# Performance work log

Measured on AMD Instinct MI355X. Metric: run time of the kernel, lower is better.

## Reference

```python
import jax, jax.numpy as jnp
import numpy as np

DIM = 1024
H = 16
DH = 64
INTER = H * DH

def setup_inputs() -> dict:
    key = jax.random.key(0)
    k1, k2, k3, k4 = jax.random.split(key, 4)
    input = jax.random.normal(k1, (4, 2048, DIM), dtype=jnp.float32)
    # nn.Linear weights stored as [out, in]; we keep [in, out] for x @ W
    W_qkv = jax.random.normal(k2, (DIM, INTER * 3), dtype=jnp.float32) * 0.02
    W_mlp = jax.random.normal(k3, (INTER, DIM), dtype=jnp.float32) * 0.02
    b_mlp = jax.random.normal(k4, (DIM,), dtype=jnp.float32) * 0.02
    return {"input": input, "W_qkv": W_qkv, "W_mlp": W_mlp, "b_mlp": b_mlp}

def reference(input, W_qkv, W_mlp, b_mlp):
    b, n, _ = input.shape
    qkv = input @ W_qkv                      # [b, n, 3*h*d]
    qkv = qkv.reshape(b, n, 3, H, DH)        # matches '(qkv h d)' split order
    qkv = jnp.transpose(qkv, (2, 0, 3, 1, 4))  # [3, b, h, n, d]
    q, k, v = qkv[0], qkv[1], qkv[2]
    scale = DH ** -0.5
    attn = jnp.einsum('bhnd,bhmd->bhnm', q, k) * scale
    attn = jax.nn.softmax(attn, axis=-1)
    out = jnp.einsum('bhnm,bhmd->bhnd', attn, v)
    out = jnp.transpose(out, (0, 2, 1, 3)).reshape(b, n, INTER)  # 'b h n d -> b n (h d)'
    return out @ W_mlp + b_mlp
```

## Files before the change

### kernel.cpp

```cpp
#include <hip/hip_runtime.h>
#include <stdint.h>

typedef __attribute__((ext_vector_type(8))) short bf16x8;
typedef __attribute__((ext_vector_type(4))) float f32x4;
typedef __attribute__((ext_vector_type(16))) float f32x16;

#define MFMA16(a, b, c) __builtin_amdgcn_mfma_f32_16x16x32_bf16((a), (b), (c), 0, 0, 0)
#define MFMA32(a, b, c) __builtin_amdgcn_mfma_f32_32x32x16_bf16((a), (b), (c), 0, 0, 0)

__device__ __forceinline__ unsigned short f2bf(float x) {
  uint32_t u = __float_as_uint(x);
  u += 0x7fffu + ((u >> 16) & 1u);
  return (unsigned short)(u >> 16);
}

__device__ __forceinline__ uint32_t cvt_pk_bf16(float a, float b) {
  uint32_t r;
  asm("v_cvt_pk_bf16_f32 %0, %1, %2" : "=v"(r) : "v"(a), "v"(b));
  return r;
}

__device__ __forceinline__ float exp2_hw(float x) {
  float r;
  asm("v_exp_f32 %0, %1" : "=v"(r) : "v"(x));
  return r;
}

__device__ __forceinline__ void gload_lds16(const void* g, void* l) {
  __builtin_amdgcn_global_load_lds(
      (const __attribute__((address_space(1))) uint32_t*)g,
      (__attribute__((address_space(3))) uint32_t*)l, 16, 0, 0);
}

__global__ __launch_bounds__(256) void prep_kernel(
    const float* __restrict__ X, unsigned short* __restrict__ Xb,
    const float* __restrict__ Wq, unsigned short* __restrict__ Wqt,
    const float* __restrict__ Wm, unsigned short* __restrict__ Wmt) {
  __shared__ float tile[64][65];
  const int bid = blockIdx.x;
  const int t = threadIdx.x;
  if (bid < 4096) {
    const int i = bid * 256 + t;
    const float4 a = *(const float4*)(X + (size_t)i * 8);
    const float4 b = *(const float4*)(X + (size_t)i * 8 + 4);
    uint4 o;
    o.x = (uint32_t)f2bf(a.x) | ((uint32_t)f2bf(a.y) << 16);
    o.y = (uint32_t)f2bf(a.z) | ((uint32_t)f2bf(a.w) << 16);
    o.z = (uint32_t)f2bf(b.x) | ((uint32_t)f2bf(b.y) << 16);
    o.w = (uint32_t)f2bf(b.z) | ((uint32_t)f2bf(b.w) << 16);
    *(uint4*)(Xb + (size_t)i * 8) = o;
    return;
  }
  const float* src;
  unsigned short* dst;
  int Nd, lb;
  if (bid < 4864) { src = Wq; dst = Wqt; Nd = 3072; lb = bid - 4096; }
  else            { src = Wm; dst = Wmt; Nd = 1024; lb = bid - 4864; }
  const int Kd = 1024;
  const int ntc = Nd >> 6;
  const int r0 = (lb / ntc) << 6;
  const int c0 = (lb % ntc) << 6;
  const int tr = t >> 4;
  const int tc4 = (t & 15) << 2;
#pragma unroll
  for (int p = 0; p < 4; ++p) {
    int row = p * 16 + tr;
    float4 v = *(const float4*)(src + (size_t)(r0 + row) * Nd + c0 + tc4);
    tile[row][tc4 + 0] = v.x;
    tile[row][tc4 + 1] = v.y;
    tile[row][tc4 + 2] = v.z;
    tile[row][tc4 + 3] = v.w;
  }
  __syncthreads();
#pragma unroll
  for (int p = 0; p < 4; ++p) {
    int c = p * 16 + tr;
    int r4 = (t & 15) << 2;
    uint2 pv;
    pv.x = (uint32_t)f2bf(tile[r4 + 0][c]) | ((uint32_t)f2bf(tile[r4 + 1][c]) << 16);
    pv.y = (uint32_t)f2bf(tile[r4 + 2][c]) | ((uint32_t)f2bf(tile[r4 + 3][c]) << 16);
    *(uint2*)(dst + (size_t)(c0 + c) * Kd + r0 + r4) = pv;
  }
}

__global__ __launch_bounds__(256) void gemm_qkv_kernel(
    const unsigned short* __restrict__ A,
    const unsigned short* __restrict__ Bt,
    unsigned short* __restrict__ Qo,
    unsigned short* __restrict__ Ko,
    unsigned short* __restrict__ Vo) {
  constexpr int Kdim = 1024, BK = 64;
  __shared__ unsigned short lA[128 * BK];
  __shared__ unsigned short lB[128 * BK];
  const int nbn = 24;
  const int wg = (blockIdx.x & 7) * 192 + (blockIdx.x >> 3);
  const int bi = wg / nbn, bj = wg % nbn;
  const int tid = threadIdx.x;
  const int l = tid & 63, w = tid >> 6;
  const int wr = w >> 1, wc = w & 1;
  const int lr = l & 15, lg = l >> 4;

  const f32x4 vzero = {0.f, 0.f, 0.f, 0.f};
  f32x4 acc[4][4];
#pragma unroll
  for (int i = 0; i < 4; ++i)
#pragma unroll
    for (int j = 0; j < 4; ++j) acc[i][j] = vzero;

  const int srow = tid >> 3;
  const int sc = tid & 7;
  const int sg = sc ^ (srow & 7);
  const unsigned short* As = A + (size_t)(bi * 128 + srow) * Kdim + sg * 8;
  const unsigned short* Bs = Bt + (size_t)(bj * 128 + srow) * Kdim + sg * 8;
  unsigned short* dA = &lA[(srow * 8 + sc) * 8];
  unsigned short* dB = &lB[(srow * 8 + sc) * 8];

  for (int kt = 0; kt < Kdim / BK; ++kt) {
    const int k0 = kt * BK;
#pragma unroll
    for (int rr = 0; rr < 4; ++rr) {
      gload_lds16(As + (size_t)rr * 32 * Kdim + k0, dA + rr * 32 * BK);
      gload_lds16(Bs + (size_t)rr * 32 * Kdim + k0, dB + rr * 32 * BK);
    }
    __syncthreads();
#pragma unroll
    for (int kk = 0; kk < 2; ++kk) {
      bf16x8 af[4], bfr[4];
#pragma unroll
      for (int it = 0; it < 4; ++it) {
        int r = wr * 64 + it * 16 + lr;
        af[it] = *(const bf16x8*)&lA[r * BK + (((kk * 4 + lg) ^ (lr & 7)) * 8)];
      }
#pragma unroll
      for (int jt = 0; jt < 4; ++jt) {
        int r = wc * 64 + jt * 16 + lr;
        bfr[jt] = *(const bf16x8*)&lB[r * BK + (((kk * 4 + lg) ^ (lr & 7)) * 8)];
      }
#pragma unroll
      for (int it = 0; it < 4; ++it)
#pragma unroll
        for (int jt = 0; jt < 4; ++jt)
          acc[it][jt] = MFMA16(af[it], bfr[jt], acc[it][jt]);
    }
    __syncthreads();
  }

#pragma unroll
  for (int jt = 0; jt < 4; ++jt) {
    const int col = bj * 128 + wc * 64 + jt * 16 + lr;
    const int s = col >> 10;
    const int rem = col & 1023;
    const int h = rem >> 6, d = rem & 63;
#pragma unroll
    for (int it = 0; it < 4; ++it) {
      const int m0 = bi * 128 + wr * 64 + it * 16 + lg * 4;
      const int b = m0 >> 11, n = m0 & 2047;
      const size_t bh = (size_t)b * 16 + h;
      if (s == 2) {
        uint2 pv;
        pv.x = (uint32_t)f2bf(acc[it][jt][0]) | ((uint32_t)f2bf(acc[it][jt][1]) << 16);
        pv.y = (uint32_t)f2bf(acc[it][jt][2]) | ((uint32_t)f2bf(acc[it][jt][3]) << 16);
        *(uint2*)(Vo + ((bh * 256 + (n >> 3)) * 64 + d) * 8 + (n & 7)) = pv;
      } else if (s == 1) {
        const size_t base = ((bh * 8 + (d >> 3)) * 2048) * 8 + (d & 7);
#pragma unroll
        for (int rg = 0; rg < 4; ++rg)
          Ko[base + (size_t)(n + rg) * 8] = f2bf(acc[it][jt][rg]);
      } else {
#pragma unroll
        for (int rg = 0; rg < 4; ++rg)
          Qo[(bh * 2048 + (size_t)(n + rg)) * 64 + d] = f2bf(acc[it][jt][rg] * 0.18033688011112042f);
      }
    }
  }
}

template <int T>
__device__ __forceinline__ bf16x8 build_pa(const f32x16& s, int hi) {
  uint32_t A1 = cvt_pk_bf16(s[T * 8 + 0], s[T * 8 + 1]);
  uint32_t A2 = cvt_pk_bf16(s[T * 8 + 2], s[T * 8 + 3]);
  uint32_t B1 = cvt_pk_bf16(s[T * 8 + 4], s[T * 8 + 5]);
  uint32_t B2 = cvt_pk_bf16(s[T * 8 + 6], s[T * 8 + 7]);
  uint32_t send1 = hi ? A1 : B1;
  uint32_t send2 = hi ? A2 : B2;
  uint32_t recv1 = (uint32_t)__shfl_xor((int)send1, 32);
  uint32_t recv2 = (uint32_t)__shfl_xor((int)send2, 32);
  union { uint32_t u[4]; bf16x8 v; } r;
  r.u[0] = hi ? recv1 : A1;
  r.u[1] = hi ? recv2 : A2;
  r.u[2] = hi ? B1 : recv1;
  r.u[3] = hi ? B2 : recv2;
  return r.v;
}

__device__ __forceinline__ float tile_sum(const f32x16& a, const f32x16& b) {
  float st[8];
#pragma unroll
  for (int i = 0; i < 8; ++i) st[i] = (a[i] + a[i + 8]) + (b[i] + b[i + 8]);
  float sm = ((st[0] + st[1]) + (st[2] + st[3])) + ((st[4] + st[5]) + (st[6] + st[7]));
  sm += __shfl_xor(sm, 32);
  return sm;
}

__global__ __launch_bounds__(256, 2) void attn_kernel(
    const unsigned short* __restrict__ Qg,
    const unsigned short* __restrict__ Kg,
    const unsigned short* __restrict__ Vg,
    unsigned short* __restrict__ AO) {
  const int bid = blockIdx.x;
  const int bh = (bid & 7) * 8 + (bid >> 6);
  const int qt = (bid >> 3) & 7;
  const int tid = threadIdx.x;
  const int l = tid & 63, w = tid >> 6;
  const int lo = l & 31, hi = l >> 5;
  const int qb = qt * 256 + w * 64;

  bf16x8 qfA[4], qfB[4];
  {
    const unsigned short* qrowA = Qg + ((size_t)bh * 2048 + qb + lo) * 64 + hi * 8;
    const unsigned short* qrowB = qrowA + 32 * 64;
#pragma unroll
    for (int ds = 0; ds < 4; ++ds) {
      qfA[ds] = *(const bf16x8*)(qrowA + ds * 16);
      qfB[ds] = *(const bf16x8*)(qrowB + ds * 16);
    }
  }

  f32x16 oA0, oA1, oB0, oB1;
#pragma unroll
  for (int i = 0; i < 16; ++i) { oA0[i] = 0.f; oA1[i] = 0.f; oB0[i] = 0.f; oB1[i] = 0.f; }
  float lA_ = 0.f, lB_ = 0.f;

  const unsigned short* Kp = Kg + ((size_t)(bh * 8 + hi) * 2048 + lo) * 8;
  const unsigned short* Vp = Vg + ((size_t)(bh * 256 + hi) * 64 + lo) * 8;

  bf16x8 kf0[4], kf1[4], vf0[4], vf1[4];
#pragma unroll
  for (int ds = 0; ds < 4; ++ds) {
    kf0[ds] = *(const bf16x8*)(Kp + ds * 32768);
    kf1[ds] = *(const bf16x8*)(Kp + ds * 32768 + 256);
  }

  for (int t = 0; t < 32; ++t) {
#pragma unroll
    for (int ks = 0; ks < 4; ++ks) {
      vf0[ks] = *(const bf16x8*)(Vp + (size_t)t * 4096 + ks * 1024);
      vf1[ks] = *(const bf16x8*)(Vp + (size_t)t * 4096 + ks * 1024 + 256);
    }

    f32x16 sA0, sA1, sB0, sB1;
#pragma unroll
    for (int i = 0; i < 16; ++i) { sA0[i] = 0.f; sA1[i] = 0.f; sB0[i] = 0.f; sB1[i] = 0.f; }
    __builtin_amdgcn_s_setprio(1);
#pragma unroll
    for (int ds = 0; ds < 4; ++ds) {
      sA0 = MFMA32(kf0[ds], qfA[ds], sA0);
      sA1 = MFMA32(kf1[ds], qfA[ds], sA1);
      sB0 = MFMA32(kf0[ds], qfB[ds], sB0);
      sB1 = MFMA32(kf1[ds], qfB[ds], sB1);
    }
    __builtin_amdgcn_s_setprio(0);

    if (t < 31) {
#pragma unroll
      for (int ds = 0; ds < 4; ++ds) {
        kf0[ds] = *(const bf16x8*)(Kp + (size_t)(t + 1) * 512 + ds * 32768);
        kf1[ds] = *(const bf16x8*)(Kp + (size_t)(t + 1) * 512 + ds * 32768 + 256);
      }
    }

#pragma unroll
    for (int i = 0; i < 16; ++i) { sA0[i] = exp2_hw(sA0[i]); sA1[i] = exp2_hw(sA1[i]); }
#pragma unroll
    for (int i = 0; i < 16; ++i) { sB0[i] = exp2_hw(sB0[i]); sB1[i] = exp2_hw(sB1[i]); }
    lA_ += tile_sum(sA0, sA1);
    lB_ += tile_sum(sB0, sB1);

    bf16x8 paA[4] = {build_pa<0>(sA0, hi), build_pa<1>(sA0, hi),
                     build_pa<0>(sA1, hi), build_pa<1>(sA1, hi)};
    bf16x8 paB[4] = {build_pa<0>(sB0, hi), build_pa<1>(sB0, hi),
                     build_pa<0>(sB1, hi), build_pa<1>(sB1, hi)};

    __builtin_amdgcn_s_setprio(1);
#pragma unroll
    for (int ks = 0; ks < 4; ++ks) {
      oA0 = MFMA32(vf0[ks], paA[ks], oA0);
      oA1 = MFMA32(vf1[ks], paA[ks], oA1);
      oB0 = MFMA32(vf0[ks], paB[ks], oB0);
      oB1 = MFMA32(vf1[ks], paB[ks], oB1);
    }
    __builtin_amdgcn_s_setprio(0);
  }

  const float linvA = 1.0f / lA_;
  const float linvB = 1.0f / lB_;
  const int b = bh >> 4, h = bh & 15;
  unsigned short* dstA = AO + ((size_t)(b * 2048 + qb + lo) * 1024 + h * 64 + 4 * hi);
  unsigned short* dstB = dstA + (size_t)32 * 1024;
#pragma unroll
  for (int q4 = 0; q4 < 4; ++q4) {
    uint2 p0;
    p0.x = cvt_pk_bf16(oA0[q4 * 4 + 0] * linvA, oA0[q4 * 4 + 1] * linvA);
    p0.y = cvt_pk_bf16(oA0[q4 * 4 + 2] * linvA, oA0[q4 * 4 + 3] * linvA);
    *(uint2*)(dstA + q4 * 8) = p0;
    uint2 p1;
    p1.x = cvt_pk_bf16(oA1[q4 * 4 + 0] * linvA, oA1[q4 * 4 + 1] * linvA);
    p1.y = cvt_pk_bf16(oA1[q4 * 4 + 2] * linvA, oA1[q4 * 4 + 3] * linvA);
    *(uint2*)(dstA + 32 + q4 * 8) = p1;
    uint2 p2;
    p2.x = cvt_pk_bf16(oB0[q4 * 4 + 0] * linvB, oB0[q4 * 4 + 1] * linvB);
    p2.y = cvt_pk_bf16(oB0[q4 * 4 + 2] * linvB, oB0[q4 * 4 + 3] * linvB);
    *(uint2*)(dstB + q4 * 8) = p2;
    uint2 p3;
    p3.x = cvt_pk_bf16(oB1[q4 * 4 + 0] * linvB, oB1[q4 * 4 + 1] * linvB);
    p3.y = cvt_pk_bf16(oB1[q4 * 4 + 2] * linvB, oB1[q4 * 4 + 3] * linvB);
    *(uint2*)(dstB + 32 + q4 * 8) = p3;
  }
}

__global__ __launch_bounds__(256) void gemm_mlp_kernel(
    const unsigned short* __restrict__ A,
    const unsigned short* __restrict__ Bt,
    const float* __restrict__ bias,
    float* __restrict__ out) {
  constexpr int Kdim = 1024, BK = 64;
  __shared__ unsigned short lA[128 * BK];
  __shared__ unsigned short lB[128 * BK];
  const int nbn = 8;
  const int wg = (blockIdx.x & 7) * 64 + (blockIdx.x >> 3);
  const int bi = wg / nbn, bj = wg % nbn;
  const int tid = threadIdx.x;
  const int l = tid & 63, w = tid >> 6;
  const int wr = w >> 1, wc = w & 1;
  const int lr = l & 15, lg = l >> 4;

  const f32x4 vzero = {0.f, 0.f, 0.f, 0.f};
  f32x4 acc[4][4];
#pragma unroll
  for (int i = 0; i < 4; ++i)
#pragma unroll
    for (int j = 0; j < 4; ++j) acc[i][j] = vzero;

  const int srow = tid >> 3;
  const int sc = tid & 7;
  const int sg = sc ^ (srow & 7);
  const unsigned short* As = A + (size_t)(bi * 128 + srow) * Kdim + sg * 8;
  const unsigned short* Bs = Bt + (size_t)(bj * 128 + srow) * Kdim + sg * 8;
  unsigned short* dA = &lA[(srow * 8 + sc) * 8];
  unsigned short* dB = &lB[(srow * 8 + sc) * 8];

  for (int kt = 0; kt < Kdim / BK; ++kt) {
    const int k0 = kt * BK;
#pragma unroll
    for (int rr = 0; rr < 4; ++rr) {
      gload_lds16(As + (size_t)rr * 32 * Kdim + k0, dA + rr * 32 * BK);
      gload_lds16(Bs + (size_t)rr * 32 * Kdim + k0, dB + rr * 32 * BK);
    }
    __syncthreads();
#pragma unroll
    for (int kk = 0; kk < 2; ++kk) {
      bf16x8 af[4], bfr[4];
#pragma unroll
      for (int it = 0; it < 4; ++it) {
        int r = wr * 64 + it * 16 + lr;
        af[it] = *(const bf16x8*)&lA[r * BK + (((kk * 4 + lg) ^ (lr & 7)) * 8)];
      }
#pragma unroll
      for (int jt = 0; jt < 4; ++jt) {
        int r = wc * 64 + jt * 16 + lr;
        bfr[jt] = *(const bf16x8*)&lB[r * BK + (((kk * 4 + lg) ^ (lr & 7)) * 8)];
      }
#pragma unroll
      for (int it = 0; it < 4; ++it)
#pragma unroll
        for (int jt = 0; jt < 4; ++jt)
          acc[it][jt] = MFMA16(af[it], bfr[jt], acc[it][jt]);
    }
    __syncthreads();
  }

#pragma unroll
  for (int jt = 0; jt < 4; ++jt) {
    const int col = bj * 128 + wc * 64 + jt * 16 + lr;
    const float bv = bias[col];
#pragma unroll
    for (int it = 0; it < 4; ++it) {
      const int m0 = bi * 128 + wr * 64 + it * 16 + lg * 4;
#pragma unroll
      for (int rg = 0; rg < 4; ++rg)
        out[(size_t)(m0 + rg) * 1024 + col] = acc[it][jt][rg] + bv;
    }
  }
}

extern "C" void kernel_launch(void* const* d_in, const int* in_sizes, int n_in,
                              void* d_out, int out_size, void* d_ws, size_t ws_size,
                              hipStream_t stream) {
  const float* X = (const float*)d_in[0];
  const float* Wqkv = (const float*)d_in[1];
  const float* Wmlp = (const float*)d_in[2];
  const float* bmlp = (const float*)d_in[3];
  float* out = (float*)d_out;

  char* ws = (char*)d_ws;
  unsigned short* Xb  = (unsigned short*)(ws);
  unsigned short* Wqt = (unsigned short*)(ws + 16777216);
  unsigned short* Wmt = (unsigned short*)(ws + 23068672);
  unsigned short* Qb  = (unsigned short*)(ws + 25165824);
  unsigned short* Kb  = (unsigned short*)(ws + 41943040);
  unsigned short* Vb  = (unsigned short*)(ws + 58720256);
  unsigned short* AOb = (unsigned short*)(ws + 75497472);

  prep_kernel<<<5120, 256, 0, stream>>>(X, Xb, Wqkv, Wqt, Wmlp, Wmt);
  gemm_qkv_kernel<<<1536, 256, 0, stream>>>(Xb, Wqt, Qb, Kb, Vb);
  attn_kernel<<<512, 256, 0, stream>>>(Qb, Kb, Vb, AOb);
  gemm_mlp_kernel<<<512, 256, 0, stream>>>(AOb, Wmt, bmlp, out);
}
```

Measured before the change: 191.5 us.

## Double-buffer QKV GEMM LDS with 128x256 tiles and 512-thread blocks

Rewrites the QKV projection GEMM to use 512-thread workgroups computing 128x256 output tiles. The K-loop is double-buffered in LDS so the global-to-LDS load of the next K slice overlaps MFMA work on the current one, and each iteration is split into two MFMA phases with barriers and s_setprio. The wider tile gives more reuse of the A tile and halves the grid. The cost is roughly 96KB of LDS per block, which limits occupancy, plus extra barriers per iteration.

```diff
diff --git a/kernel.cpp b/kernel.cpp
--- a/kernel.cpp
+++ b/kernel.cpp
@@ -83,21 +83,21 @@
   }
 }
 
-__global__ __launch_bounds__(256) void gemm_qkv_kernel(
+__global__ __launch_bounds__(512, 2) void gemm_qkv_kernel(
     const unsigned short* __restrict__ A,
     const unsigned short* __restrict__ Bt,
     unsigned short* __restrict__ Qo,
     unsigned short* __restrict__ Ko,
     unsigned short* __restrict__ Vo) {
   constexpr int Kdim = 1024, BK = 64;
-  __shared__ unsigned short lA[128 * BK];
-  __shared__ unsigned short lB[128 * BK];
-  const int nbn = 24;
-  const int wg = (blockIdx.x & 7) * 192 + (blockIdx.x >> 3);
+  __shared__ unsigned short lA[2][128 * BK];
+  __shared__ unsigned short lB[2][256 * BK];
+  const int nbn = 12;
+  const int wg = (blockIdx.x & 7) * 96 + (blockIdx.x >> 3);
   const int bi = wg / nbn, bj = wg % nbn;
   const int tid = threadIdx.x;
-  const int l = tid & 63, w = tid >> 6;
-  const int wr = w >> 1, wc = w & 1;
+  const int l = tid & 63, wid = tid >> 6;
+  const int wr = wid >> 2, wc = wid & 3;
   const int lr = l & 15, lg = l >> 4;
 
   const f32x4 vzero = {0.f, 0.f, 0.f, 0.f};
@@ -111,43 +111,82 @@
   const int sc = tid & 7;
   const int sg = sc ^ (srow & 7);
   const unsigned short* As = A + (size_t)(bi * 128 + srow) * Kdim + sg * 8;
-  const unsigned short* Bs = Bt + (size_t)(bj * 128 + srow) * Kdim + sg * 8;
-  unsigned short* dA = &lA[(srow * 8 + sc) * 8];
-  unsigned short* dB = &lB[(srow * 8 + sc) * 8];
-
-  for (int kt = 0; kt < Kdim / BK; ++kt) {
-    const int k0 = kt * BK;
-#pragma unroll
-    for (int rr = 0; rr < 4; ++rr) {
-      gload_lds16(As + (size_t)rr * 32 * Kdim + k0, dA + rr * 32 * BK);
-      gload_lds16(Bs + (size_t)rr * 32 * Kdim + k0, dB + rr * 32 * BK);
-    }
-    __syncthreads();
-#pragma unroll
-    for (int kk = 0; kk < 2; ++kk) {
-      bf16x8 af[4], bfr[4];
-#pragma unroll
-      for (int it = 0; it < 4; ++it) {
-        int r = wr * 64 + it * 16 + lr;
-        af[it] = *(const bf16x8*)&lA[r * BK + (((kk * 4 + lg) ^ (lr & 7)) * 8)];
-      }
+  const unsigned short* Bs = Bt + (size_t)(bj * 256 + srow) * Kdim + sg * 8;
+
+#define STAGE_T(nb, kt)                                                          \
+  {                                                                              \
+    const int k0_ = (kt) * BK;                                                   \
+    gload_lds16(As + k0_,                    &lA[nb][(srow) * BK + sc * 8]);     \
+    gload_lds16(As + (size_t)64 * Kdim + k0_, &lA[nb][(srow + 64) * BK + sc * 8]);\
+    gload_lds16(Bs + k0_,                    &lB[nb][(srow) * BK + sc * 8]);     \
+    gload_lds16(Bs + (size_t)64 * Kdim + k0_, &lB[nb][(srow + 64) * BK + sc * 8]);\
+    gload_lds16(Bs + (size_t)128 * Kdim + k0_, &lB[nb][(srow + 128) * BK + sc * 8]);\
+    gload_lds16(Bs + (size_t)192 * Kdim + k0_, &lB[nb][(srow + 192) * BK + sc * 8]);\
+  }
+
+  STAGE_T(0, 0);
+  asm volatile("s_waitcnt vmcnt(0)" ::: "memory");
+  __builtin_amdgcn_s_barrier();
+
+  for (int T = 0; T < 16; ++T) {
+    const int cur = T & 1;
+    bf16x8 bfr[4][2], af[2][2];
+#pragma unroll
+    for (int jt = 0; jt < 4; ++jt) {
+      const int r = wc * 64 + jt * 16 + lr;
+#pragma unroll
+      for (int kk = 0; kk < 2; ++kk)
+        bfr[jt][kk] = *(const bf16x8*)&lB[cur][r * BK + (((kk * 4 + lg) ^ (r & 7)) * 8)];
+    }
+#pragma unroll
+    for (int it = 0; it < 2; ++it) {
+      const int r = wr * 64 + it * 16 + lr;
+#pragma unroll
+      for (int kk = 0; kk < 2; ++kk)
+        af[it][kk] = *(const bf16x8*)&lA[cur][r * BK + (((kk * 4 + lg) ^ (r & 7)) * 8)];
+    }
+    if (T < 15) STAGE_T(cur ^ 1, T + 1);
+    __builtin_amdgcn_s_barrier();
+    asm volatile("s_waitcnt lgkmcnt(0)" ::: "memory");
+    __builtin_amdgcn_sched_barrier(0);
+    __builtin_amdgcn_s_setprio(1);
+#pragma unroll
+    for (int it = 0; it < 2; ++it)
 #pragma unroll
       for (int jt = 0; jt < 4; ++jt) {
-        int r = wc * 64 + jt * 16 + lr;
-        bfr[jt] = *(const bf16x8*)&lB[r * BK + (((kk * 4 + lg) ^ (lr & 7)) * 8)];
-      }
-#pragma unroll
-      for (int it = 0; it < 4; ++it)
-#pragma unroll
-        for (int jt = 0; jt < 4; ++jt)
-          acc[it][jt] = MFMA16(af[it], bfr[jt], acc[it][jt]);
-    }
-    __syncthreads();
+        acc[it][jt] = MFMA16(af[it][0], bfr[jt][0], acc[it][jt]);
+        acc[it][jt] = MFMA16(af[it][1], bfr[jt][1], acc[it][jt]);
+      }
+    __builtin_amdgcn_s_setprio(0);
+    __builtin_amdgcn_s_barrier();
+
+    bf16x8 af2[2][2];
+#pragma unroll
+    for (int it = 0; it < 2; ++it) {
+      const int r = wr * 64 + (it + 2) * 16 + lr;
+#pragma unroll
+      for (int kk = 0; kk < 2; ++kk)
+        af2[it][kk] = *(const bf16x8*)&lA[cur][r * BK + (((kk * 4 + lg) ^ (r & 7)) * 8)];
+    }
+    __builtin_amdgcn_s_barrier();
+    asm volatile("s_waitcnt lgkmcnt(0)" ::: "memory");
+    __builtin_amdgcn_sched_barrier(0);
+    __builtin_amdgcn_s_setprio(1);
+#pragma unroll
+    for (int it = 0; it < 2; ++it)
+#pragma unroll
+      for (int jt = 0; jt < 4; ++jt) {
+        acc[it + 2][jt] = MFMA16(af2[it][0], bfr[jt][0], acc[it + 2][jt]);
+        acc[it + 2][jt] = MFMA16(af2[it][1], bfr[jt][1], acc[it + 2][jt]);
+      }
+    __builtin_amdgcn_s_setprio(0);
+    asm volatile("s_waitcnt vmcnt(0)" ::: "memory");
+    __builtin_amdgcn_s_barrier();
   }
 
 #pragma unroll
   for (int jt = 0; jt < 4; ++jt) {
-    const int col = bj * 128 + wc * 64 + jt * 16 + lr;
+    const int col = bj * 256 + wc * 64 + jt * 16 + lr;
     const int s = col >> 10;
     const int rem = col & 1023;
     const int h = rem >> 6, d = rem & 63;
@@ -173,6 +212,7 @@
       }
     }
   }
+#undef STAGE_T
 }
 
 template <int T>
@@ -412,7 +452,7 @@
   unsigned short* AOb = (unsigned short*)(ws + 75497472);
 
   prep_kernel<<<5120, 256, 0, stream>>>(X, Xb, Wqkv, Wqt, Wmlp, Wmt);
-  gemm_qkv_kernel<<<1536, 256, 0, stream>>>(Xb, Wqt, Qb, Kb, Vb);
+  gemm_qkv_kernel<<<768, 512, 0, stream>>>(Xb, Wqt, Qb, Kb, Vb);
   attn_kernel<<<512, 256, 0, stream>>>(Qb, Kb, Vb, AOb);
   gemm_mlp_kernel<<<512, 256, 0, stream>>>(AOb, Wmt, bmlp, out);
 }
```

Result: no change. 191.3 us (-0.1%).
